# Kernel tuning notes

Hardware: AMD Instinct MI355X
Metric: run time of the kernel (lower is better)

## Reference

```python
import jax, jax.numpy as jnp
import numpy as np
from jax.ops import segment_sum, segment_max

N = 50000          # nodes
E = 1_600_000      # edges (before self-loops)
IN = 16            # in_channels
F = 20             # N_features
H1 = 4             # heads in conv1
EDGE_DIM = 7
OUT = 3            # out_channels
NEG_SLOPE = 0.2


def setup_inputs() -> dict:
    key = jax.random.key(0)
    ks = jax.random.split(key, 24)
    g = lambda k, shape, fan: (jax.random.normal(k, shape, jnp.float32)
                               * (1.0 / np.sqrt(fan)))
    inp = {}
    inp["x"] = jax.random.normal(ks[0], (N, IN), jnp.float32)
    inp["edge_index"] = jax.random.randint(ks[1], (2, E), 0, N, jnp.int32)
    inp["edge_attr"] = jax.random.normal(ks[2], (E, EDGE_DIM), jnp.float32)
    # conv1: IN -> F, heads=H1, edge_dim=EDGE_DIM
    inp["W1"] = g(ks[3], (IN, H1 * F), IN)
    inp["att_src1"] = g(ks[4], (H1, F), F)
    inp["att_dst1"] = g(ks[5], (H1, F), F)
    inp["We1"] = g(ks[6], (EDGE_DIM, H1 * F), EDGE_DIM)
    inp["att_e1"] = g(ks[7], (H1, F), F)
    inp["b1"] = jnp.zeros((H1 * F,), jnp.float32)
    # conv2: (H1*F) -> F, heads=1, edge_dim=EDGE_DIM
    inp["W2"] = g(ks[8], (H1 * F, F), H1 * F)
    inp["att_src2"] = g(ks[9], (1, F), F)
    inp["att_dst2"] = g(ks[10], (1, F), F)
    inp["We2"] = g(ks[11], (EDGE_DIM, F), EDGE_DIM)
    inp["att_e2"] = g(ks[12], (1, F), F)
    inp["b2"] = jnp.zeros((F,), jnp.float32)
    # decoder: F -> 10 -> OUT
    inp["D1w"] = g(ks[13], (F, 10), F)
    inp["D1b"] = jnp.zeros((10,), jnp.float32)
    inp["D2w"] = g(ks[14], (10, OUT), 10)
    inp["D2b"] = jnp.zeros((OUT,), jnp.float32)
    return inp


def _gat_layer(x, src, dst, eattr, W, a_s, a_d, We, a_e, b, heads, fdim):
    """PyG GATConv (shared src/dst lin, add_self_loops already applied)."""
    n = x.shape[0]
    xh = (x @ W).reshape(n, heads, fdim)                  # [N,H,F]
    eh = (eattr @ We).reshape(-1, heads, fdim)            # [Ea,H,F]
    a_src = jnp.sum(xh * a_s, axis=-1)                    # [N,H]
    a_dst = jnp.sum(xh * a_d, axis=-1)                    # [N,H]
    a_edge = jnp.sum(eh * a_e, axis=-1)                   # [Ea,H]
    logits = a_src[src] + a_dst[dst] + a_edge             # [Ea,H]
    logits = jnp.where(logits >= 0, logits, NEG_SLOPE * logits)
    # segment softmax over destination node
    m = segment_max(logits, dst, num_segments=n)          # [N,H]
    ex = jnp.exp(logits - m[dst])
    denom = segment_sum(ex, dst, num_segments=n)          # [N,H]
    alpha = ex / (denom[dst] + 1e-16)                     # [Ea,H]
    msg = xh[src] * alpha[:, :, None]                     # [Ea,H,F]
    out = segment_sum(msg, dst, num_segments=n)           # [N,H,F]
    return out.reshape(n, heads * fdim) + b


def reference(x, edge_index, edge_attr, W1, att_src1, att_dst1, We1, att_e1,
              b1, W2, att_src2, att_dst2, We2, att_e2, b2, D1w, D1b, D2w, D2b):
    src, dst = edge_index[0], edge_index[1]
    # add self-loops with edge_attr fill_value='mean' (scatter-mean by dst)
    deg = segment_sum(jnp.ones((E,), jnp.float32), dst, num_segments=N)
    mean_attr = segment_sum(edge_attr, dst, num_segments=N) \
        / jnp.maximum(deg, 1.0)[:, None]
    loops = jnp.arange(N, dtype=src.dtype)
    src_a = jnp.concatenate([src, loops])
    dst_a = jnp.concatenate([dst, loops])
    eattr_a = jnp.concatenate([edge_attr, mean_attr], axis=0)
    # conv1 (heads=4, concat) -> elu  (dropouts are no-ops in eval)
    h = _gat_layer(x, src_a, dst_a, eattr_a, W1, att_src1, att_dst1,
                   We1, att_e1, b1, H1, F)
    h = jax.nn.elu(h)
    # conv2 (heads=1) -> elu
    h = _gat_layer(h, src_a, dst_a, eattr_a, W2, att_src2, att_dst2,
                   We2, att_e2, b2, 1, F)
    h = jax.nn.elu(h)
    # decoder MLP
    h = jax.nn.relu(h @ D1w + D1b)
    return h @ D2w + D2b
```

## Files before the change

kernel.cpp:

```cpp
#include <hip/hip_runtime.h>
#include <hip/hip_fp16.h>

constexpr int NN  = 50000;
constexpr int EEg = 1600000;
constexpr int IND = 16;
constexpr int FD  = 20;
constexpr int H1D = 4;
constexpr int ED  = 7;
constexpr int OUTD = 3;
constexpr int FP  = 24;

__device__ __forceinline__ float lrelu(float x) { return x >= 0.0f ? x : 0.2f * x; }
__device__ __forceinline__ float elu(float x)   { return x > 0.0f ? x : expm1f(x); }
__device__ __forceinline__ unsigned pack2(float a, float b) {
    __half2 h = __floats2half2_rn(a, b);
    return *(unsigned*)&h;
}
__device__ __forceinline__ float2 up2(unsigned w) {
    __half2 h = *(__half2*)&w;
    return __half22float2(h);
}

__global__ void k_deg(const int* __restrict__ ei, int* __restrict__ deg,
                      int* __restrict__ rank) {
    int e = blockIdx.x * blockDim.x + threadIdx.x;
    if (e >= EEg) return;
    rank[e] = atomicAdd(&deg[ei[EEg + e]], 1);
}

__global__ void k_ve(const float* __restrict__ We1, const float* __restrict__ ae1,
                     const float* __restrict__ We2, const float* __restrict__ ae2,
                     float* __restrict__ ve1, float* __restrict__ ve2) {
    int t = threadIdx.x;
    if (t < ED * H1D) {
        int d = t >> 2, h = t & 3;
        float s = 0.0f;
        for (int f = 0; f < FD; ++f) s += We1[d * (H1D * FD) + h * FD + f] * ae1[h * FD + f];
        ve1[t] = s;
    } else if (t < ED * H1D + ED) {
        int d = t - ED * H1D;
        float s = 0.0f;
        for (int f = 0; f < FD; ++f) s += We2[d * FD + f] * ae2[f];
        ve2[d] = s;
    }
}

__global__ void k_scanA(const int* __restrict__ deg, int* __restrict__ partial,
                        int* __restrict__ bsum) {
    __shared__ int sd[256];
    int t = threadIdx.x, i = blockIdx.x * 256 + t;
    int v = (i < NN) ? deg[i] : 0;
    sd[t] = v;
    __syncthreads();
    for (int off = 1; off < 256; off <<= 1) {
        int u = (t >= off) ? sd[t - off] : 0;
        __syncthreads();
        sd[t] += u;
        __syncthreads();
    }
    if (i < NN) partial[i] = sd[t] - v;
    if (t == 255) bsum[blockIdx.x] = sd[255];
}
__global__ void k_scanB(const int* __restrict__ bsum, int* __restrict__ boff, int nb) {
    __shared__ int sd[256];
    int t = threadIdx.x;
    int v = (t < nb) ? bsum[t] : 0;
    sd[t] = v;
    __syncthreads();
    for (int off = 1; off < 256; off <<= 1) {
        int u = (t >= off) ? sd[t - off] : 0;
        __syncthreads();
        sd[t] += u;
        __syncthreads();
    }
    if (t < nb) boff[t] = sd[t] - v;
}
__global__ void k_scanC(const int* __restrict__ partial, const int* __restrict__ boff,
                        int* __restrict__ row_off) {
    int i = blockIdx.x * 256 + threadIdx.x;
    if (i < NN) row_off[i] = partial[i] + boff[blockIdx.x];
    if (i == 0) row_off[NN] = EEg;
}

__global__ void k_scatter(const int* __restrict__ ei, const float* __restrict__ eattr,
                          const float* __restrict__ ve1, const float* __restrict__ ve2,
                          const int* __restrict__ row_off, const int* __restrict__ rank,
                          uint4* __restrict__ csr) {
    __shared__ float sv1[ED * H1D], sv2[ED];
    if (threadIdx.x < ED * H1D) sv1[threadIdx.x] = ve1[threadIdx.x];
    if (threadIdx.x < ED) sv2[threadIdx.x] = ve2[threadIdx.x];
    __syncthreads();
    int e = blockIdx.x * blockDim.x + threadIdx.x;
    if (e >= EEg) return;
    int src = ei[e], dst = ei[EEg + e];
    float a[ED];
#pragma unroll
    for (int d = 0; d < ED; ++d) a[d] = eattr[e * ED + d];
    float v0 = 0.f, v1 = 0.f, v2 = 0.f, v3 = 0.f, w2 = 0.f;
#pragma unroll
    for (int d = 0; d < ED; ++d) {
        v0 += a[d] * sv1[d * H1D + 0];
        v1 += a[d] * sv1[d * H1D + 1];
        v2 += a[d] * sv1[d * H1D + 2];
        v3 += a[d] * sv1[d * H1D + 3];
        w2 += a[d] * sv2[d];
    }
    int slot = row_off[dst] + rank[e];
    uint4 rec;
    rec.x = (unsigned)src;
    rec.y = pack2(v0, v1);
    rec.z = pack2(v2, v3);
    rec.w = pack2(w2, 0.0f);
    csr[slot] = rec;
}

__global__ void k_mean_self(const int* __restrict__ row_off, const uint4* __restrict__ csr,
                            float* __restrict__ a_e1s, float* __restrict__ a_e2s) {
    int n = blockIdx.x * blockDim.x + threadIdx.x;
    if (n >= NN) return;
    int beg = row_off[n], end = row_off[n + 1];
    float s0 = 0.f, s1 = 0.f, s2 = 0.f, s3 = 0.f, se = 0.f;
    for (int j = beg; j < end; ++j) {
        uint4 r = csr[j];
        float2 a01 = up2(r.y), a23 = up2(r.z), ap = up2(r.w);
        s0 += a01.x; s1 += a01.y; s2 += a23.x; s3 += a23.y; se += ap.x;
    }
    float inv = 1.0f / fmaxf((float)(end - beg), 1.0f);
    a_e1s[n * H1D + 0] = s0 * inv;
    a_e1s[n * H1D + 1] = s1 * inv;
    a_e1s[n * H1D + 2] = s2 * inv;
    a_e1s[n * H1D + 3] = s3 * inv;
    a_e2s[n] = se * inv;
}

__global__ void k_xh1attn1(const float* __restrict__ x, const float* __restrict__ W1,
                           const float* __restrict__ as, const float* __restrict__ ad,
                           __half* __restrict__ xh1h, float* __restrict__ a_src1,
                           float* __restrict__ a_dst1) {
    __shared__ float sW[IND * H1D * FD];
    for (int i = threadIdx.x; i < IND * H1D * FD; i += blockDim.x) sW[i] = W1[i];
    __syncthreads();
    int idx = blockIdx.x * blockDim.x + threadIdx.x;
    if (idx >= NN * H1D) return;
    int n = idx >> 2, h = idx & 3;
    float xr[IND];
    const float4* xp = (const float4*)&x[(size_t)n * IND];
#pragma unroll
    for (int q = 0; q < IND / 4; ++q) {
        float4 v = xp[q];
        xr[4 * q] = v.x; xr[4 * q + 1] = v.y; xr[4 * q + 2] = v.z; xr[4 * q + 3] = v.w;
    }
    float ss = 0.f, sd = 0.f;
    float o[FD];
#pragma unroll
    for (int f = 0; f < FD; ++f) {
        float s = 0.f;
#pragma unroll
        for (int k = 0; k < IND; ++k) s += xr[k] * sW[k * (H1D * FD) + h * FD + f];
        o[f] = s;
        ss += s * as[h * FD + f];
        sd += s * ad[h * FD + f];
    }
    uint4* xo = (uint4*)&xh1h[((size_t)n * H1D + h) * FP];
    xo[0] = make_uint4(pack2(o[0], o[1]), pack2(o[2], o[3]), pack2(o[4], o[5]), pack2(o[6], o[7]));
    xo[1] = make_uint4(pack2(o[8], o[9]), pack2(o[10], o[11]), pack2(o[12], o[13]), pack2(o[14], o[15]));
    xo[2] = make_uint4(pack2(o[16], o[17]), pack2(o[18], o[19]), 0u, 0u);
    a_src1[idx] = ss; a_dst1[idx] = sd;
}

#define GATHER_ACC(ex, base)                                            \
    {                                                                   \
        const uint4* xr_ = (const uint4*)(base);                        \
        uint4 g0 = xr_[0], g1 = xr_[1];                                 \
        uint2 g2 = *(const uint2*)(xr_ + 2);                            \
        float2 f_;                                                      \
        f_ = up2(g0.x); acc[0] += (ex) * f_.x;  acc[1] += (ex) * f_.y;  \
        f_ = up2(g0.y); acc[2] += (ex) * f_.x;  acc[3] += (ex) * f_.y;  \
        f_ = up2(g0.z); acc[4] += (ex) * f_.x;  acc[5] += (ex) * f_.y;  \
        f_ = up2(g0.w); acc[6] += (ex) * f_.x;  acc[7] += (ex) * f_.y;  \
        f_ = up2(g1.x); acc[8] += (ex) * f_.x;  acc[9] += (ex) * f_.y;  \
        f_ = up2(g1.y); acc[10] += (ex) * f_.x; acc[11] += (ex) * f_.y; \
        f_ = up2(g1.z); acc[12] += (ex) * f_.x; acc[13] += (ex) * f_.y; \
        f_ = up2(g1.w); acc[14] += (ex) * f_.x; acc[15] += (ex) * f_.y; \
        f_ = up2(g2.x); acc[16] += (ex) * f_.x; acc[17] += (ex) * f_.y; \
        f_ = up2(g2.y); acc[18] += (ex) * f_.x; acc[19] += (ex) * f_.y; \
    }

__global__ __launch_bounds__(64) void k_conv1(
        const int* __restrict__ row_off, const uint4* __restrict__ csr,
        const float* __restrict__ a_src1, const float* __restrict__ a_dst1,
        const float* __restrict__ a_e1s, const __half* __restrict__ xh1h,
        const float* __restrict__ b1, float* __restrict__ h1) {
    int idx = blockIdx.x * 64 + threadIdx.x;
    int n = idx >> 3, h = idx & 3, p = (idx >> 2) & 1;
    int beg = row_off[n], end = row_off[n + 1];
    float adst = a_dst1[n * H1D + h];
    float m, denom;
    float acc[FD];
    if (p == 0) {
        m = lrelu(a_src1[n * H1D + h] + adst + a_e1s[n * H1D + h]);
        denom = 1.0f;
#pragma unroll
        for (int f = 0; f < FD; ++f) acc[f] = 0.f;
        GATHER_ACC(1.0f, &xh1h[((size_t)n * H1D + h) * FP]);
    } else {
        m = -1e30f; denom = 0.f;
#pragma unroll
        for (int f = 0; f < FD; ++f) acc[f] = 0.f;
    }
    for (int j = beg + p; j < end; j += 2) {
        uint4 r = csr[j];
        int s = (int)r.x;
        unsigned w = (h < 2) ? r.y : r.z;
        float2 aep = up2(w);
        float ae = (h & 1) ? aep.y : aep.x;
        float l = lrelu(a_src1[s * H1D + h] + adst + ae);
        if (l > m) {
            float sc = expf(m - l);
            denom *= sc;
#pragma unroll
            for (int f = 0; f < FD; ++f) acc[f] *= sc;
            m = l;
        }
        float ex = expf(l - m);
        denom += ex;
        GATHER_ACC(ex, &xh1h[((size_t)s * H1D + h) * FP]);
    }
    float mo = __shfl_xor(m, 4);
    float dno = __shfl_xor(denom, 4);
    float M = fmaxf(m, mo);
    float ssf = expf(m - M), sof = expf(mo - M);
    denom = denom * ssf + dno * sof;
#pragma unroll
    for (int f = 0; f < FD; ++f) acc[f] = acc[f] * ssf + __shfl_xor(acc[f], 4) * sof;
    if (p) return;
    float inv = 1.0f / (denom + 1e-16f);
    float* ho = &h1[((size_t)n * H1D + h) * FD];
#pragma unroll
    for (int f = 0; f < FD; ++f) ho[f] = elu(acc[f] * inv + b1[h * FD + f]);
}

__global__ void k_xh2attn2(const float* __restrict__ h1, const float* __restrict__ W2,
                           const float* __restrict__ as, const float* __restrict__ ad,
                           __half* __restrict__ xh2h, float* __restrict__ a_src2,
                           float* __restrict__ a_dst2) {
    __shared__ float sW[H1D * FD * FD];
    for (int i = threadIdx.x; i < H1D * FD * FD; i += blockDim.x) sW[i] = W2[i];
    __syncthreads();
    int n = blockIdx.x * blockDim.x + threadIdx.x;
    if (n >= NN) return;
    float hr[H1D * FD];
    const float4* hp = (const float4*)&h1[(size_t)n * (H1D * FD)];
#pragma unroll
    for (int q = 0; q < (H1D * FD) / 4; ++q) {
        float4 v = hp[q];
        hr[4 * q] = v.x; hr[4 * q + 1] = v.y; hr[4 * q + 2] = v.z; hr[4 * q + 3] = v.w;
    }
    float ss = 0.f, sd = 0.f;
    float o[FD];
#pragma unroll
    for (int f = 0; f < FD; ++f) {
        float s = 0.f;
#pragma unroll
        for (int k = 0; k < H1D * FD; ++k) s += hr[k] * sW[k * FD + f];
        o[f] = s;
        ss += s * as[f];
        sd += s * ad[f];
    }
    uint4* xo = (uint4*)&xh2h[(size_t)n * FP];
    xo[0] = make_uint4(pack2(o[0], o[1]), pack2(o[2], o[3]), pack2(o[4], o[5]), pack2(o[6], o[7]));
    xo[1] = make_uint4(pack2(o[8], o[9]), pack2(o[10], o[11]), pack2(o[12], o[13]), pack2(o[14], o[15]));
    xo[2] = make_uint4(pack2(o[16], o[17]), pack2(o[18], o[19]), 0u, 0u);
    a_src2[n] = ss; a_dst2[n] = sd;
}

__global__ __launch_bounds__(64) void k_conv2dec(
        const int* __restrict__ row_off, const uint4* __restrict__ csr,
        const float* __restrict__ a_src2, const float* __restrict__ a_dst2,
        const float* __restrict__ a_e2s, const __half* __restrict__ xh2h,
        const float* __restrict__ b2, const float* __restrict__ D1w,
        const float* __restrict__ D1b, const float* __restrict__ D2w,
        const float* __restrict__ D2b, float* __restrict__ out) {
    __shared__ float sD1w[FD * 10], sD1b[10], sD2w[10 * OUTD], sD2b[OUTD], sb2[FD];
    for (int i = threadIdx.x; i < FD * 10; i += blockDim.x) sD1w[i] = D1w[i];
    if (threadIdx.x < 10) sD1b[threadIdx.x] = D1b[threadIdx.x];
    if (threadIdx.x < 10 * OUTD) sD2w[threadIdx.x] = D2w[threadIdx.x];
    if (threadIdx.x < OUTD) sD2b[threadIdx.x] = D2b[threadIdx.x];
    if (threadIdx.x < FD) sb2[threadIdx.x] = b2[threadIdx.x];
    __syncthreads();
    int idx = blockIdx.x * 64 + threadIdx.x;
    if (idx >= NN * 2) return;
    int n = idx >> 1, p = idx & 1;
    int beg = row_off[n], end = row_off[n + 1];
    float adst = a_dst2[n];
    float m, denom;
    float acc[FD];
    if (p == 0) {
        m = lrelu(a_src2[n] + adst + a_e2s[n]);
        denom = 1.0f;
#pragma unroll
        for (int f = 0; f < FD; ++f) acc[f] = 0.f;
        GATHER_ACC(1.0f, &xh2h[(size_t)n * FP]);
    } else {
        m = -1e30f; denom = 0.f;
#pragma unroll
        for (int f = 0; f < FD; ++f) acc[f] = 0.f;
    }
    for (int j = beg + p; j < end; j += 2) {
        uint4 r = csr[j];
        int s = (int)r.x;
        float l = lrelu(a_src2[s] + adst + up2(r.w).x);
        if (l > m) {
            float sc = expf(m - l);
            denom *= sc;
#pragma unroll
            for (int f = 0; f < FD; ++f) acc[f] *= sc;
            m = l;
        }
        float ex = expf(l - m);
        denom += ex;
        GATHER_ACC(ex, &xh2h[(size_t)s * FP]);
    }
    float mo = __shfl_xor(m, 1);
    float dno = __shfl_xor(denom, 1);
    float M = fmaxf(m, mo);
    float ssf = expf(m - M), sof = expf(mo - M);
    denom = denom * ssf + dno * sof;
#pragma unroll
    for (int f = 0; f < FD; ++f) acc[f] = acc[f] * ssf + __shfl_xor(acc[f], 1) * sof;
    if (p) return;
    float inv = 1.0f / (denom + 1e-16f);
    float h2[FD];
#pragma unroll
    for (int f = 0; f < FD; ++f) h2[f] = elu(acc[f] * inv + sb2[f]);
    float o[OUTD];
#pragma unroll
    for (int k = 0; k < OUTD; ++k) o[k] = sD2b[k];
    for (int j = 0; j < 10; ++j) {
        float hid = sD1b[j];
#pragma unroll
        for (int f = 0; f < FD; ++f) hid += h2[f] * sD1w[f * 10 + j];
        hid = fmaxf(hid, 0.0f);
#pragma unroll
        for (int k = 0; k < OUTD; ++k) o[k] += hid * sD2w[j * OUTD + k];
    }
#pragma unroll
    for (int k = 0; k < OUTD; ++k) out[n * OUTD + k] = o[k];
}

extern "C" void kernel_launch(void* const* d_in, const int* in_sizes, int n_in,
                              void* d_out, int out_size, void* d_ws, size_t ws_size,
                              hipStream_t stream) {
    const float* x     = (const float*)d_in[0];
    const int*   ei    = (const int*)d_in[1];
    const float* eattr = (const float*)d_in[2];
    const float* W1    = (const float*)d_in[3];
    const float* as1   = (const float*)d_in[4];
    const float* ad1   = (const float*)d_in[5];
    const float* We1   = (const float*)d_in[6];
    const float* ae1   = (const float*)d_in[7];
    const float* b1    = (const float*)d_in[8];
    const float* W2    = (const float*)d_in[9];
    const float* as2   = (const float*)d_in[10];
    const float* ad2   = (const float*)d_in[11];
    const float* We2   = (const float*)d_in[12];
    const float* ae2   = (const float*)d_in[13];
    const float* b2    = (const float*)d_in[14];
    const float* D1w   = (const float*)d_in[15];
    const float* D1b   = (const float*)d_in[16];
    const float* D2w   = (const float*)d_in[17];
    const float* D2b   = (const float*)d_in[18];
    float* out = (float*)d_out;

    float* w = (float*)d_ws;
    size_t o = 0;
    int*   deg = (int*)(w + o); o += NN;
    size_t zero_bytes = o * sizeof(float);
    int*   rank    = (int*)(w + o); o += EEg;
    int*   partial = (int*)(w + o); o += NN;
    int*   bsum    = (int*)(w + o); o += 256;
    int*   boff    = (int*)(w + o); o += 256;
    int*   row_off = (int*)(w + o); o += NN + 4;
    float* csr     = w + o; o += (size_t)EEg * 4;
    float* ve1     = w + o; o += 32;
    float* ve2     = w + o; o += 8;
    float* a_e1s   = w + o; o += (size_t)NN * H1D;
    float* a_e2s   = w + o; o += NN;
    float* a_src1  = w + o; o += (size_t)NN * H1D;
    float* a_dst1  = w + o; o += (size_t)NN * H1D;
    __half* xh1h   = (__half*)(w + o); o += (size_t)NN * H1D * FP / 2;
    float* h1      = w + o; o += (size_t)NN * H1D * FD;
    __half* xh2h   = (__half*)(w + o); o += (size_t)NN * FP / 2;
    float* a_src2  = w + o; o += NN;
    float* a_dst2  = w + o; o += NN;

    hipMemsetAsync(d_ws, 0, zero_bytes, stream);

    const int B = 256;
    auto cdiv = [](long a, long b) { return (int)((a + b - 1) / b); };
    const int NB = cdiv(NN, 256);

    k_deg<<<cdiv(EEg, B), B, 0, stream>>>(ei, deg, rank);
    k_ve<<<1, 64, 0, stream>>>(We1, ae1, We2, ae2, ve1, ve2);
    k_scanA<<<NB, 256, 0, stream>>>(deg, partial, bsum);
    k_scanB<<<1, 256, 0, stream>>>(bsum, boff, NB);
    k_scanC<<<NB, 256, 0, stream>>>(partial, boff, row_off);
    k_scatter<<<cdiv(EEg, B), B, 0, stream>>>(ei, eattr, ve1, ve2, row_off, rank,
                                              (uint4*)csr);
    k_mean_self<<<cdiv(NN, B), B, 0, stream>>>(row_off, (const uint4*)csr, a_e1s, a_e2s);
    k_xh1attn1<<<cdiv((long)NN * H1D, B), B, 0, stream>>>(x, W1, as1, ad1, xh1h, a_src1,
                                                          a_dst1);
    k_conv1<<<NN * 8 / 64, 64, 0, stream>>>(row_off, (const uint4*)csr, a_src1, a_dst1,
                                            a_e1s, xh1h, b1, h1);
    k_xh2attn2<<<cdiv(NN, B), B, 0, stream>>>(h1, W2, as2, ad2, xh2h, a_src2, a_dst2);
    k_conv2dec<<<cdiv((long)NN * 2, 64), 64, 0, stream>>>(row_off, (const uint4*)csr,
                                                          a_src2, a_dst2, a_e2s, xh2h, b2,
                                                          D1w, D1b, D2w, D2b, out);
}
```

Measured before the change: 280.8 us.

## Split edge aggregation across four lanes per node with software-prefetched gathers

Both GAT aggregation kernels now give each destination node (and head) four cooperating lanes instead of two, and combine the partial online-softmax states with a two-step butterfly shuffle. The loop is software-pipelined: the next edge's CSR record, source attention score and feature payload are loaded before the current edge is processed, to hide gather latency. Block size grows from 64 to 256, and expf is replaced with the faster __expf intrinsic. The extra lanes raise register use and add merge overhead, and __expf slightly lowers accuracy.

```diff
diff --git a/kernel.cpp b/kernel.cpp
--- a/kernel.cpp
+++ b/kernel.cpp
@@ -168,11 +168,8 @@
     a_src1[idx] = ss; a_dst1[idx] = sd;
 }
 
-#define GATHER_ACC(ex, base)                                            \
+#define FMA_PAYLOAD(ex, g0, g1, g2)                                     \
     {                                                                   \
-        const uint4* xr_ = (const uint4*)(base);                        \
-        uint4 g0 = xr_[0], g1 = xr_[1];                                 \
-        uint2 g2 = *(const uint2*)(xr_ + 2);                            \
         float2 f_;                                                      \
         f_ = up2(g0.x); acc[0] += (ex) * f_.x;  acc[1] += (ex) * f_.y;  \
         f_ = up2(g0.y); acc[2] += (ex) * f_.x;  acc[3] += (ex) * f_.y;  \
@@ -186,53 +183,75 @@
         f_ = up2(g2.y); acc[18] += (ex) * f_.x; acc[19] += (ex) * f_.y; \
     }
 
-__global__ __launch_bounds__(64) void k_conv1(
+__global__ __launch_bounds__(256) void k_conv1(
         const int* __restrict__ row_off, const uint4* __restrict__ csr,
         const float* __restrict__ a_src1, const float* __restrict__ a_dst1,
         const float* __restrict__ a_e1s, const __half* __restrict__ xh1h,
         const float* __restrict__ b1, float* __restrict__ h1) {
-    int idx = blockIdx.x * 64 + threadIdx.x;
-    int n = idx >> 3, h = idx & 3, p = (idx >> 2) & 1;
+    int idx = blockIdx.x * 256 + threadIdx.x;
+    int n = idx >> 4, low = idx & 15, h = low & 3, p = low >> 2;
     int beg = row_off[n], end = row_off[n + 1];
     float adst = a_dst1[n * H1D + h];
     float m, denom;
     float acc[FD];
+#pragma unroll
+    for (int f = 0; f < FD; ++f) acc[f] = 0.f;
     if (p == 0) {
         m = lrelu(a_src1[n * H1D + h] + adst + a_e1s[n * H1D + h]);
         denom = 1.0f;
-#pragma unroll
-        for (int f = 0; f < FD; ++f) acc[f] = 0.f;
-        GATHER_ACC(1.0f, &xh1h[((size_t)n * H1D + h) * FP]);
+        const uint4* xp = (const uint4*)&xh1h[((size_t)n * H1D + h) * FP];
+        uint4 s0 = xp[0], s1 = xp[1];
+        uint2 s2 = *(const uint2*)(xp + 2);
+        FMA_PAYLOAD(1.0f, s0, s1, s2);
     } else {
         m = -1e30f; denom = 0.f;
-#pragma unroll
-        for (int f = 0; f < FD; ++f) acc[f] = 0.f;
-    }
-    for (int j = beg + p; j < end; j += 2) {
-        uint4 r = csr[j];
+    }
+    int j = beg + p;
+    uint4 r; float av; uint4 g0, g1; uint2 g2;
+    if (j < end) {
+        r = csr[j];
         int s = (int)r.x;
-        unsigned w = (h < 2) ? r.y : r.z;
-        float2 aep = up2(w);
+        av = a_src1[s * H1D + h];
+        const uint4* xp = (const uint4*)&xh1h[((size_t)s * H1D + h) * FP];
+        g0 = xp[0]; g1 = xp[1]; g2 = *(const uint2*)(xp + 2);
+    }
+    while (j < end) {
+        int jn = j + 4;
+        uint4 rn; float avn; uint4 n0, n1; uint2 n2;
+        if (jn < end) {
+            rn = csr[jn];
+            int sn = (int)rn.x;
+            avn = a_src1[sn * H1D + h];
+            const uint4* xp = (const uint4*)&xh1h[((size_t)sn * H1D + h) * FP];
+            n0 = xp[0]; n1 = xp[1]; n2 = *(const uint2*)(xp + 2);
+        }
+        unsigned wae = (h < 2) ? r.y : r.z;
+        float2 aep = up2(wae);
         float ae = (h & 1) ? aep.y : aep.x;
-        float l = lrelu(a_src1[s * H1D + h] + adst + ae);
+        float l = lrelu(av + adst + ae);
         if (l > m) {
-            float sc = expf(m - l);
+            float sc = __expf(m - l);
             denom *= sc;
 #pragma unroll
             for (int f = 0; f < FD; ++f) acc[f] *= sc;
             m = l;
         }
-        float ex = expf(l - m);
+        float ex = __expf(l - m);
         denom += ex;
-        GATHER_ACC(ex, &xh1h[((size_t)s * H1D + h) * FP]);
-    }
-    float mo = __shfl_xor(m, 4);
-    float dno = __shfl_xor(denom, 4);
-    float M = fmaxf(m, mo);
-    float ssf = expf(m - M), sof = expf(mo - M);
-    denom = denom * ssf + dno * sof;
-#pragma unroll
-    for (int f = 0; f < FD; ++f) acc[f] = acc[f] * ssf + __shfl_xor(acc[f], 4) * sof;
+        FMA_PAYLOAD(ex, g0, g1, g2);
+        j = jn; r = rn; av = avn; g0 = n0; g1 = n1; g2 = n2;
+    }
+#pragma unroll
+    for (int st = 4; st <= 8; st <<= 1) {
+        float mo = __shfl_xor(m, st);
+        float dno = __shfl_xor(denom, st);
+        float M = fmaxf(m, mo);
+        float ssf = __expf(m - M), sof = __expf(mo - M);
+        denom = denom * ssf + dno * sof;
+#pragma unroll
+        for (int f = 0; f < FD; ++f) acc[f] = acc[f] * ssf + __shfl_xor(acc[f], st) * sof;
+        m = M;
+    }
     if (p) return;
     float inv = 1.0f / (denom + 1e-16f);
     float* ho = &h1[((size_t)n * H1D + h) * FD];
@@ -274,7 +293,7 @@
     a_src2[n] = ss; a_dst2[n] = sd;
 }
 
-__global__ __launch_bounds__(64) void k_conv2dec(
+__global__ __launch_bounds__(256) void k_conv2dec(
         const int* __restrict__ row_off, const uint4* __restrict__ csr,
         const float* __restrict__ a_src2, const float* __restrict__ a_dst2,
         const float* __restrict__ a_e2s, const __half* __restrict__ xh2h,
@@ -288,46 +307,68 @@
     if (threadIdx.x < OUTD) sD2b[threadIdx.x] = D2b[threadIdx.x];
     if (threadIdx.x < FD) sb2[threadIdx.x] = b2[threadIdx.x];
     __syncthreads();
-    int idx = blockIdx.x * 64 + threadIdx.x;
-    if (idx >= NN * 2) return;
-    int n = idx >> 1, p = idx & 1;
+    int idx = blockIdx.x * 256 + threadIdx.x;
+    if (idx >= NN * 4) return;
+    int n = idx >> 2, p = idx & 3;
     int beg = row_off[n], end = row_off[n + 1];
     float adst = a_dst2[n];
     float m, denom;
     float acc[FD];
+#pragma unroll
+    for (int f = 0; f < FD; ++f) acc[f] = 0.f;
     if (p == 0) {
         m = lrelu(a_src2[n] + adst + a_e2s[n]);
         denom = 1.0f;
-#pragma unroll
-        for (int f = 0; f < FD; ++f) acc[f] = 0.f;
-        GATHER_ACC(1.0f, &xh2h[(size_t)n * FP]);
+        const uint4* xp = (const uint4*)&xh2h[(size_t)n * FP];
+        uint4 s0 = xp[0], s1 = xp[1];
+        uint2 s2 = *(const uint2*)(xp + 2);
+        FMA_PAYLOAD(1.0f, s0, s1, s2);
     } else {
         m = -1e30f; denom = 0.f;
-#pragma unroll
-        for (int f = 0; f < FD; ++f) acc[f] = 0.f;
-    }
-    for (int j = beg + p; j < end; j += 2) {
-        uint4 r = csr[j];
+    }
+    int j = beg + p;
+    uint4 r; float av; uint4 g0, g1; uint2 g2;
+    if (j < end) {
+        r = csr[j];
         int s = (int)r.x;
-        float l = lrelu(a_src2[s] + adst + up2(r.w).x);
+        av = a_src2[s];
+        const uint4* xp = (const uint4*)&xh2h[(size_t)s * FP];
+        g0 = xp[0]; g1 = xp[1]; g2 = *(const uint2*)(xp + 2);
+    }
+    while (j < end) {
+        int jn = j + 4;
+        uint4 rn; float avn; uint4 n0, n1; uint2 n2;
+        if (jn < end) {
+            rn = csr[jn];
+            int sn = (int)rn.x;
+            avn = a_src2[sn];
+            const uint4* xp = (const uint4*)&xh2h[(size_t)sn * FP];
+            n0 = xp[0]; n1 = xp[1]; n2 = *(const uint2*)(xp + 2);
+        }
+        float l = lrelu(av + adst + up2(r.w).x);
         if (l > m) {
-            float sc = expf(m - l);
+            float sc = __expf(m - l);
             denom *= sc;
 #pragma unroll
             for (int f = 0; f < FD; ++f) acc[f] *= sc;
             m = l;
         }
-        float ex = expf(l - m);
+        float ex = __expf(l - m);
         denom += ex;
-        GATHER_ACC(ex, &xh2h[(size_t)s * FP]);
-    }
-    float mo = __shfl_xor(m, 1);
-    float dno = __shfl_xor(denom, 1);
-    float M = fmaxf(m, mo);
-    float ssf = expf(m - M), sof = expf(mo - M);
-    denom = denom * ssf + dno * sof;
-#pragma unroll
-    for (int f = 0; f < FD; ++f) acc[f] = acc[f] * ssf + __shfl_xor(acc[f], 1) * sof;
+        FMA_PAYLOAD(ex, g0, g1, g2);
+        j = jn; r = rn; av = avn; g0 = n0; g1 = n1; g2 = n2;
+    }
+#pragma unroll
+    for (int st = 1; st <= 2; st <<= 1) {
+        float mo = __shfl_xor(m, st);
+        float dno = __shfl_xor(denom, st);
+        float M = fmaxf(m, mo);
+        float ssf = __expf(m - M), sof = __expf(mo - M);
+        denom = denom * ssf + dno * sof;
+#pragma unroll
+        for (int f = 0; f < FD; ++f) acc[f] = acc[f] * ssf + __shfl_xor(acc[f], st) * sof;
+        m = M;
+    }
     if (p) return;
     float inv = 1.0f / (denom + 1e-16f);
     float h2[FD];
@@ -336,13 +377,13 @@
     float o[OUTD];
 #pragma unroll
     for (int k = 0; k < OUTD; ++k) o[k] = sD2b[k];
-    for (int j = 0; j < 10; ++j) {
-        float hid = sD1b[j];
-#pragma unroll
-        for (int f = 0; f < FD; ++f) hid += h2[f] * sD1w[f * 10 + j];
+    for (int j2 = 0; j2 < 10; ++j2) {
+        float hid = sD1b[j2];
+#pragma unroll
+        for (int f = 0; f < FD; ++f) hid += h2[f] * sD1w[f * 10 + j2];
         hid = fmaxf(hid, 0.0f);
 #pragma unroll
-        for (int k = 0; k < OUTD; ++k) o[k] += hid * sD2w[j * OUTD + k];
+        for (int k = 0; k < OUTD; ++k) o[k] += hid * sD2w[j2 * OUTD + k];
     }
 #pragma unroll
     for (int k = 0; k < OUTD; ++k) out[n * OUTD + k] = o[k];
@@ -410,10 +451,11 @@
     k_mean_self<<<cdiv(NN, B), B, 0, stream>>>(row_off, (const uint4*)csr, a_e1s, a_e2s);
     k_xh1attn1<<<cdiv((long)NN * H1D, B), B, 0, stream>>>(x, W1, as1, ad1, xh1h, a_src1,
                                                           a_dst1);
-    k_conv1<<<NN * 8 / 64, 64, 0, stream>>>(row_off, (const uint4*)csr, a_src1, a_dst1,
-                                            a_e1s, xh1h, b1, h1);
+    k_conv1<<<cdiv((long)NN * 16, 256), 256, 0, stream>>>(row_off, (const uint4*)csr,
+                                                          a_src1, a_dst1, a_e1s, xh1h, b1,
+                                                          h1);
     k_xh2attn2<<<cdiv(NN, B), B, 0, stream>>>(h1, W2, as2, ad2, xh2h, a_src2, a_dst2);
-    k_conv2dec<<<cdiv((long)NN * 2, 64), 64, 0, stream>>>(row_off, (const uint4*)csr,
-                                                          a_src2, a_dst2, a_e2s, xh2h, b2,
-                                                          D1w, D1b, D2w, D2b, out);
-}
+    k_conv2dec<<<cdiv((long)NN * 4, 256), 256, 0, stream>>>(row_off, (const uint4*)csr,
+                                                            a_src2, a_dst2, a_e2s, xh2h,
+                                                            b2, D1w, D1b, D2w, D2b, out);
+}
```

Result: no change. 283.1 us (+0.8%).
